# Performance work log

Measured on AMD Instinct MI355X. Metric: run time of the kernel, lower is better.

The kernel has to match this reference:

```python
import jax, jax.numpy as jnp
import numpy as np

# static config (matches init_kwargs)
B, HID, NH, D = 1, 1024, 16, 64
T, Hh, W = 8, 32, 32
TT, TH, TW = 2, 8, 8            # tile sizes (numel 128)
WT, WH, WW = 6 // TT, 16 // TH, 16 // TW  # window in tiles: 3,2,2
NTT, NTH, NTW = T // TT, Hh // TH, W // TW  # 4,4,4
NTILE = NTT * NTH * NTW          # 64
TILE = TT * TH * TW              # 128
WK = WT * WH * WW                # 12 kv tiles per q tile
S = T * Hh * W


def _dim_window(nt, w):
    left = w // 2
    right = w // 2 + (w % 2) - 1
    center = jnp.clip(jnp.arange(nt), left, nt - 1 - right)
    return center[:, None] - left + jnp.arange(w)  # [nt, w]


def _kv_tile_idx():
    kt = _dim_window(NTT, WT)  # [NTT, WT]
    kh = _dim_window(NTH, WH)  # [NTH, WH]
    kw = _dim_window(NTW, WW)  # [NTW, WW]
    idx = (kt[:, None, None, :, None, None] * (NTH * NTW)
           + kh[None, :, None, None, :, None] * NTW
           + kw[None, None, :, None, None, :])
    return idx.reshape(NTILE, WK)


def _to_tiles(x, nh):
    # [B, S, nh*D] -> [B, nh, NTILE, TILE, D]; seq laid out (ntt tt nth th ntw tw)
    x = x.reshape(B, NTT, TT, NTH, TH, NTW, TW, nh, D)
    x = x.transpose(0, 7, 1, 3, 5, 2, 4, 6, 8)
    return x.reshape(B, nh, NTILE, TILE, D)


def _from_tiles(o):
    # [B, NH, NTILE, TILE, D] -> [B, S, NH*D]
    o = o.reshape(B, NH, NTT, NTH, NTW, TT, TH, TW, D)
    o = o.transpose(0, 2, 5, 3, 6, 4, 7, 1, 8)
    return o.reshape(B, S, NH * D)


def setup_inputs() -> dict:
    key = jax.random.key(0)
    ks = jax.random.split(key, 5)
    sc = 1.0 / np.sqrt(HID)
    return {
        'hidden_states': jax.random.normal(ks[0], (B, S, HID), jnp.float32),
        'wq': jax.random.normal(ks[1], (HID, NH * D), jnp.float32) * sc,
        'wk': jax.random.normal(ks[2], (HID, NH * D), jnp.float32) * sc,
        'wv': jax.random.normal(ks[3], (HID, NH * D), jnp.float32) * sc,
        'wo': jax.random.normal(ks[4], (NH * D, HID), jnp.float32) * sc,
    }


def reference(hidden_states, wq, wk, wv, wo):
    kv_idx = _kv_tile_idx()  # [NTILE, WK]
    q = _to_tiles(hidden_states @ wq, NH)  # [B,NH,NTILE,TILE,D]
    k = _to_tiles(hidden_states @ wk, NH)
    v = _to_tiles(hidden_states @ wv, NH)
    # gather each query tile's exact kv window (mask fully satisfied by construction)
    kg = k[:, :, kv_idx].reshape(B, NH, NTILE, WK * TILE, D)
    vg = v[:, :, kv_idx].reshape(B, NH, NTILE, WK * TILE, D)
    scores = jnp.einsum('bhnqd,bhnkd->bhnqk', q, kg) * (1.0 / np.sqrt(D))
    p = jax.nn.softmax(scores, axis=-1)
    o = jnp.einsum('bhnqk,bhnkd->bhnqd', p, vg)
    return _from_tiles(o) @ wo
```

## Files before the change

kernel.cpp:

```cpp
#include <hip/hip_runtime.h>
#include <hip/hip_bf16.h>
#include <math.h>

typedef __attribute__((ext_vector_type(8))) short          short8;
typedef __attribute__((ext_vector_type(8))) unsigned short u16x8;
typedef __attribute__((ext_vector_type(2))) unsigned int   u32x2;
typedef __attribute__((ext_vector_type(4))) float          f32x4;

#define MFMA_BF16(a, b, c) __builtin_amdgcn_mfma_f32_16x16x32_bf16((a), (b), (c), 0, 0, 0)

#define GLOAD_LDS16(gp, lp)                                        \
  __builtin_amdgcn_global_load_lds(                                \
      (const __attribute__((address_space(1))) void*)(gp),         \
      (__attribute__((address_space(3))) void*)(lp), 16, 0, 0)


__device__ __forceinline__ unsigned short f2bf(float f) {
  union { float f; unsigned int u; } v; v.f = f;
  unsigned int r = v.u + 0x7fffu + ((v.u >> 16) & 1u);
  return (unsigned short)(r >> 16);
}
__device__ __forceinline__ unsigned int pack2bf(float a, float b) {
  union { float f; unsigned int u; } x, y; x.f = a; y.f = b;
  return ((x.u + 0x8000u) >> 16) | ((y.u + 0x8000u) & 0xffff0000u);
}

__device__ __forceinline__ int row_to_seq(int r) {
  int tile = r >> 7, pos = r & 127;
  int ntt = tile >> 4, nth = (tile >> 2) & 3, ntw = tile & 3;
  int tt  = pos >> 6,  th  = (pos >> 3) & 7,  tw  = pos & 7;
  return ((ntt * 2 + tt) << 10) | ((nth * 8 + th) << 5) | (ntw * 8 + tw);
}

__global__ __launch_bounds__(256) void permute_hs(const float* __restrict__ in,
                                                  unsigned short* __restrict__ out) {
  int cid = blockIdx.x * 256 + threadIdx.x;
  int r = cid >> 7, c = (cid & 127) * 8;
  int s = row_to_seq(r);
  const float* f = in + (size_t)s * 1024 + c;
  u16x8 v;
#pragma unroll
  for (int j = 0; j < 8; ++j) v[j] = f2bf(f[j]);
  *(u16x8*)(out + (size_t)r * 1024 + c) = v;
}

__global__ __launch_bounds__(256) void transpose_w(const float* __restrict__ w0,
                                                   const float* __restrict__ w1,
                                                   const float* __restrict__ w2,
                                                   const float* __restrict__ w3,
                                                   unsigned short* __restrict__ out) {
  __shared__ unsigned short Lt[64 * 68];
  int m = blockIdx.y;
  const float* W = (m == 0) ? w0 : (m == 1) ? w1 : (m == 2) ? w2 : w3;
  unsigned short* O = out + (size_t)m * 1048576;
  int k0 = (blockIdx.x >> 4) * 64, n0 = (blockIdx.x & 15) * 64;
  int tid = threadIdx.x;
#pragma unroll
  for (int i = 0; i < 2; ++i) {
    int cid = i * 256 + tid;
    int kr = cid >> 3, c = cid & 7;
    const float* f = W + (size_t)(k0 + kr) * 1024 + n0 + c * 8;
#pragma unroll
    for (int j = 0; j < 8; ++j) Lt[(c * 8 + j) * 68 + kr] = f2bf(f[j]);
  }
  __syncthreads();
#pragma unroll
  for (int i = 0; i < 2; ++i) {
    int cid = i * 256 + tid;
    int nr = cid >> 3, c = cid & 7;
    u16x8 v;
#pragma unroll
    for (int j = 0; j < 8; ++j) v[j] = Lt[nr * 68 + c * 8 + j];
    *(u16x8*)(O + (size_t)(n0 + nr) * 1024 + k0 + c * 8) = v;
  }
}

template <int SCATTER, int OUT_F32>
__device__ __forceinline__ void gemm_bt_body(const unsigned short* __restrict__ A,
                                             const unsigned short* __restrict__ Bt,
                                             void* __restrict__ Cv,
                                             int row0, int col0, float scale) {
  __shared__ unsigned short As[128 * 64];
  __shared__ unsigned short Bs[128 * 64];
  const int tid  = threadIdx.x;
  const int lane = tid & 63, w = tid >> 6;
  const int quad = lane >> 4, lm = lane & 15;
  const int wr = (w >> 1) * 64, wc = (w & 1) * 64;
  f32x4 acc[4][4] = {};
  for (int kt = 0; kt < 16; ++kt) {
    const int k0 = kt * 64;
    __syncthreads();
#pragma unroll
    for (int i = 0; i < 4; ++i) {
      int cid = i * 256 + tid;
      int r = cid >> 3, c = cid & 7;
      int cg = c ^ (r & 7);
      int base = (i * 256 + (tid & 192)) * 8;
      GLOAD_LDS16(A  + (size_t)(row0 + r) * 1024 + k0 + cg * 8, As + base);
      GLOAD_LDS16(Bt + (size_t)(col0 + r) * 1024 + k0 + cg * 8, Bs + base);
    }
    __syncthreads();
#pragma unroll
    for (int kh = 0; kh < 2; ++kh) {
      short8 af[4], bf[4];
#pragma unroll
      for (int t = 0; t < 4; ++t) {
        int ca = (kh * 4 + quad) ^ (lm & 7);
        af[t] = *(const short8*)(As + (wr + t * 16 + lm) * 64 + ca * 8);
        bf[t] = *(const short8*)(Bs + (wc + t * 16 + lm) * 64 + ca * 8);
      }
#pragma unroll
      for (int rt = 0; rt < 4; ++rt)
#pragma unroll
        for (int ct = 0; ct < 4; ++ct)
          acc[rt][ct] = MFMA_BF16(af[rt], bf[ct], acc[rt][ct]);
    }
  }
#pragma unroll
  for (int rt = 0; rt < 4; ++rt)
#pragma unroll
    for (int ct = 0; ct < 4; ++ct)
#pragma unroll
      for (int g = 0; g < 4; ++g) {
        int R  = row0 + wr + rt * 16 + quad * 4 + g;
        int Cc = col0 + wc + ct * 16 + lm;
        int Rs = SCATTER ? row_to_seq(R) : R;
        float vv = acc[rt][ct][g] * scale;
        if (OUT_F32) ((float*)Cv)[(size_t)Rs * 1024 + Cc] = vv;
        else ((unsigned short*)Cv)[(size_t)Rs * 1024 + Cc] = f2bf(vv);
      }
}

__global__ __launch_bounds__(256) void gemm_qkv(const unsigned short* __restrict__ A,
                                                const unsigned short* __restrict__ Wt,
                                                unsigned short* __restrict__ QKV) {
  float scale = (blockIdx.z == 0) ? 0.18033688011112042f : 1.0f;
  gemm_bt_body<0, 0>(A, Wt + (size_t)blockIdx.z * 1048576,
                     QKV + (size_t)blockIdx.z * 8388608,
                     blockIdx.y * 128, blockIdx.x * 128, scale);
}

__global__ __launch_bounds__(256) void gemm_out(const unsigned short* __restrict__ A,
                                                const unsigned short* __restrict__ Wt,
                                                float* __restrict__ Cout) {
  gemm_bt_body<1, 1>(A, Wt, Cout, blockIdx.y * 128, blockIdx.x * 128, 1.0f);
}

__global__ __launch_bounds__(256) void transpose_v(const unsigned short* __restrict__ V,
                                                   unsigned short* __restrict__ Vt) {
  __shared__ unsigned short Lt[64 * 136];
  int kt = blockIdx.x, h = blockIdx.y, tid = threadIdx.x;
#pragma unroll
  for (int i = 0; i < 4; ++i) {
    int cid = i * 256 + tid;
    int r = cid >> 3, c = cid & 7;
    u16x8 v = *(const u16x8*)(V + (size_t)(kt * 128 + r) * 1024 + h * 64 + c * 8);
#pragma unroll
    for (int j = 0; j < 8; ++j) Lt[(c * 8 + j) * 136 + r] = v[j];
  }
  __syncthreads();
#pragma unroll
  for (int i = 0; i < 4; ++i) {
    int cid = i * 256 + tid;
    int d = cid >> 4, c = cid & 15;
    u16x8 v = *(const u16x8*)(Lt + d * 136 + c * 8);
    *(u16x8*)(Vt + (size_t)(h * 64 + d) * 8192 + kt * 128 + c * 8) = v;
  }
}

__global__ __launch_bounds__(512, 4) void attn(const unsigned short* __restrict__ Q,
                                               const unsigned short* __restrict__ K,
                                               const unsigned short* __restrict__ Vt,
                                               unsigned short* __restrict__ O) {
  __shared__ unsigned short Ks[128 * 64];
  __shared__ unsigned short Vs[64 * 128];
  __shared__ unsigned short Pb[8 * 16 * 64];

  const int tid  = threadIdx.x;
  const int lane = tid & 63, w = tid >> 6;
  const int quad = lane >> 4, lm = lane & 15;
  unsigned short* Pbw = Pb + w * 1024;

  const int h = blockIdx.x >> 6, qt = blockIdx.x & 63;
  const int ntt = qt >> 4, nth = (qt >> 2) & 3, ntw = qt & 3;
  const int kt0 = min(max(ntt, 1), 2) - 1;
  const int kh0 = min(max(nth, 1), 3) - 1;
  const int kw0 = min(max(ntw, 1), 3) - 1;

  short8 bq[2];
#pragma unroll
  for (int kh = 0; kh < 2; ++kh)
    bq[kh] = *(const short8*)(Q + (size_t)(qt * 128 + w * 16 + lm) * 1024
                                + h * 64 + kh * 32 + quad * 8);

  short8 ones8;
#pragma unroll
  for (int j = 0; j < 8; ++j) ones8[j] = (short)0x3F80;

  f32x4 o_acc[4] = {};
  f32x4 l_acc = {};

  {
    const int kvt0 = kt0 * 16 + kh0 * 4 + kw0;
#pragma unroll
    for (int i = 0; i < 2; ++i) {
      int cid = i * 512 + tid;
      int r = cid >> 3, c = cid & 7, cg = c ^ (r & 7);
      int base = (i * 512 + (tid & 448)) * 8;
      GLOAD_LDS16(K + (size_t)(kvt0 * 128 + r) * 1024 + h * 64 + cg * 8, Ks + base);
    }
  }
  __syncthreads();

  for (int it = 0; it < 12; ++it) {
    const int tt2 = it >> 2, hh2 = (it >> 1) & 1, ww2 = it & 1;
    const int kvt = (kt0 + tt2) * 16 + (kh0 + hh2) * 4 + (kw0 + ww2);

#pragma unroll
    for (int i = 0; i < 2; ++i) {
      int cid = i * 512 + tid;
      int d = cid >> 4, c = cid & 15, cg = c ^ (d & 7);
      int base = (i * 512 + (tid & 448)) * 8;
      GLOAD_LDS16(Vt + (size_t)(h * 64 + d) * 8192 + kvt * 128 + cg * 8, Vs + base);
    }

    f32x4 sa[8] = {};
#pragma unroll
    for (int kh = 0; kh < 2; ++kh) {
      short8 ak[8];
#pragma unroll
      for (int rt = 0; rt < 8; ++rt)
        ak[rt] = *(const short8*)(Ks + (rt * 16 + lm) * 64 + (((kh * 4 + quad) ^ (lm & 7)) * 8));
#pragma unroll
      for (int rt = 0; rt < 8; ++rt)
        sa[rt] = MFMA_BF16(ak[rt], bq[kh], sa[rt]);
    }

    u32x2 pk[8];
#pragma unroll
    for (int rt = 0; rt < 8; ++rt) {
      pk[rt][0] = pack2bf(exp2f(sa[rt][0]), exp2f(sa[rt][1]));
      pk[rt][1] = pack2bf(exp2f(sa[rt][2]), exp2f(sa[rt][3]));
    }

    __syncthreads();

    if (it < 11) {
      const int jt = it + 1;
      const int t2 = jt >> 2, h2 = (jt >> 1) & 1, w2 = jt & 1;
      const int kvn = (kt0 + t2) * 16 + (kh0 + h2) * 4 + (kw0 + w2);
#pragma unroll
      for (int i = 0; i < 2; ++i) {
        int cid = i * 512 + tid;
        int r = cid >> 3, c = cid & 7, cg = c ^ (r & 7);
        int base = (i * 512 + (tid & 448)) * 8;
        GLOAD_LDS16(K + (size_t)(kvn * 128 + r) * 1024 + h * 64 + cg * 8, Ks + base);
      }
    }

#pragma unroll
    for (int half = 0; half < 2; ++half) {
#pragma unroll
      for (int rt4 = 0; rt4 < 4; ++rt4) {
        *(u32x2*)(Pbw + lm * 64 + (((rt4 * 2 + (quad >> 1)) ^ (lm & 7)) * 8) + (quad & 1) * 4)
            = pk[half * 4 + rt4];
      }
#pragma unroll
      for (int ks2 = 0; ks2 < 2; ++ks2) {
        short8 ap = *(const short8*)(Pbw + lm * 64 + (((ks2 * 4 + quad) ^ (lm & 7)) * 8));
        l_acc = MFMA_BF16(ap, ones8, l_acc);
        const int ks = half * 2 + ks2;
#pragma unroll
        for (int nt = 0; nt < 4; ++nt) {
          short8 bv = *(const short8*)(Vs + (nt * 16 + lm) * 128 + (((ks * 4 + quad) ^ (lm & 7)) * 8));
          o_acc[nt] = MFMA_BF16(ap, bv, o_acc[nt]);
        }
      }
    }

    __syncthreads();
  }

#pragma unroll
  for (int g = 0; g < 4; ++g) {
    float inv = 1.0f / l_acc[g];
#pragma unroll
    for (int nt = 0; nt < 4; ++nt) {
      int R = qt * 128 + w * 16 + quad * 4 + g;
      O[(size_t)R * 1024 + h * 64 + nt * 16 + lm] = f2bf(o_acc[nt][g] * inv);
    }
  }
}

extern "C" void kernel_launch(void* const* d_in, const int* in_sizes, int n_in,
                              void* d_out, int out_size, void* d_ws, size_t ws_size,
                              hipStream_t stream) {
  const float* hs = (const float*)d_in[0];
  const float* wq = (const float*)d_in[1];
  const float* wk = (const float*)d_in[2];
  const float* wv = (const float*)d_in[3];
  const float* wo = (const float*)d_in[4];
  float* out = (float*)d_out;

  const size_t NEL = 8388608;
  unsigned short* ws  = (unsigned short*)d_ws;
  unsigned short* HSt = ws;
  unsigned short* Qb  = ws + 1 * NEL;
  unsigned short* Kb  = ws + 2 * NEL;
  unsigned short* Vb  = ws + 3 * NEL;
  unsigned short* Vtb = ws + 4 * NEL;
  unsigned short* Ot  = ws + 5 * NEL;
  unsigned short* Wt  = ws + 6 * NEL;
  if (ws_size < (6 * NEL + 4 * 1048576) * sizeof(unsigned short)) return;

  permute_hs<<<4096, 256, 0, stream>>>(hs, HSt);
  transpose_w<<<dim3(256, 4), 256, 0, stream>>>(wq, wk, wv, wo, Wt);
  gemm_qkv<<<dim3(8, 64, 3), 256, 0, stream>>>(HSt, Wt, Qb);
  transpose_v<<<dim3(64, 16), 256, 0, stream>>>(Vb, Vtb);
  attn<<<1024, 512, 0, stream>>>(Qb, Kb, Vtb, Ot);
  gemm_out<<<dim3(8, 64, 1), 256, 0, stream>>>(Ot, Wt + 3 * 1048576, out);
  (void)in_sizes; (void)n_in; (void)out_size;
}
```

Before: 293.1 us.

## Use hardware bf16 pack, precompute load offsets, add MFMA priority hints

Replaces the manual float-to-bf16 packing with the v_cvt_pk_bf16_f32 instruction. Global-to-LDS load addresses for K and Vt are hoisted into per-thread offsets computed once, so the loop adds only a shifted tile index. s_setprio hints are wrapped around the MFMA issues so that waves doing matrix math get scheduling priority. The packing instruction rounds differently from the old add-0x8000 truncation, and the fine-grained setprio toggles may disturb the instruction schedule.

```diff
diff --git a/kernel.cpp b/kernel.cpp
--- a/kernel.cpp
+++ b/kernel.cpp
@@ -21,8 +21,9 @@
   return (unsigned short)(r >> 16);
 }
 __device__ __forceinline__ unsigned int pack2bf(float a, float b) {
-  union { float f; unsigned int u; } x, y; x.f = a; y.f = b;
-  return ((x.u + 0x8000u) >> 16) | ((y.u + 0x8000u) & 0xffff0000u);
+  unsigned int r;
+  asm("v_cvt_pk_bf16_f32 %0, %1, %2" : "=v"(r) : "v"(a), "v"(b));
+  return r;
 }
 
 __device__ __forceinline__ int row_to_seq(int r) {
@@ -187,6 +188,18 @@
   const int kh0 = min(max(nth, 1), 3) - 1;
   const int kw0 = min(max(ntw, 1), 3) - 1;
 
+  const int cid1 = 512 + tid;
+  const int rK0 = tid  >> 3, cgK0 = (tid  & 7) ^ (rK0 & 7);
+  const int rK1 = cid1 >> 3, cgK1 = (cid1 & 7) ^ (rK1 & 7);
+  const unsigned koff0 = rK0 * 1024 + h * 64 + cgK0 * 8;
+  const unsigned koff1 = rK1 * 1024 + h * 64 + cgK1 * 8;
+  const int dV0 = tid  >> 4, cgV0 = (tid  & 15) ^ (dV0 & 7);
+  const int dV1 = cid1 >> 4, cgV1 = (cid1 & 15) ^ (dV1 & 7);
+  const unsigned voff0 = (h * 64 + dV0) * 8192 + cgV0 * 8;
+  const unsigned voff1 = (h * 64 + dV1) * 8192 + cgV1 * 8;
+  const unsigned ldsD0 = (tid & 448) * 8;
+  const unsigned ldsD1 = (512 + (tid & 448)) * 8;
+
   short8 bq[2];
 #pragma unroll
   for (int kh = 0; kh < 2; ++kh)
@@ -201,14 +214,9 @@
   f32x4 l_acc = {};
 
   {
-    const int kvt0 = kt0 * 16 + kh0 * 4 + kw0;
-#pragma unroll
-    for (int i = 0; i < 2; ++i) {
-      int cid = i * 512 + tid;
-      int r = cid >> 3, c = cid & 7, cg = c ^ (r & 7);
-      int base = (i * 512 + (tid & 448)) * 8;
-      GLOAD_LDS16(K + (size_t)(kvt0 * 128 + r) * 1024 + h * 64 + cg * 8, Ks + base);
-    }
+    const unsigned k0 = (unsigned)(kt0 * 16 + kh0 * 4 + kw0) << 17;
+    GLOAD_LDS16(K + koff0 + k0, Ks + ldsD0);
+    GLOAD_LDS16(K + koff1 + k0, Ks + ldsD1);
   }
   __syncthreads();
 
@@ -216,12 +224,10 @@
     const int tt2 = it >> 2, hh2 = (it >> 1) & 1, ww2 = it & 1;
     const int kvt = (kt0 + tt2) * 16 + (kh0 + hh2) * 4 + (kw0 + ww2);
 
-#pragma unroll
-    for (int i = 0; i < 2; ++i) {
-      int cid = i * 512 + tid;
-      int d = cid >> 4, c = cid & 15, cg = c ^ (d & 7);
-      int base = (i * 512 + (tid & 448)) * 8;
-      GLOAD_LDS16(Vt + (size_t)(h * 64 + d) * 8192 + kvt * 128 + cg * 8, Vs + base);
+    {
+      const unsigned v0 = (unsigned)kvt << 7;
+      GLOAD_LDS16(Vt + voff0 + v0, Vs + ldsD0);
+      GLOAD_LDS16(Vt + voff1 + v0, Vs + ldsD1);
     }
 
     f32x4 sa[8] = {};
@@ -231,9 +237,11 @@
 #pragma unroll
       for (int rt = 0; rt < 8; ++rt)
         ak[rt] = *(const short8*)(Ks + (rt * 16 + lm) * 64 + (((kh * 4 + quad) ^ (lm & 7)) * 8));
+      __builtin_amdgcn_s_setprio(1);
 #pragma unroll
       for (int rt = 0; rt < 8; ++rt)
         sa[rt] = MFMA_BF16(ak[rt], bq[kh], sa[rt]);
+      __builtin_amdgcn_s_setprio(0);
     }
 
     u32x2 pk[8];
@@ -248,14 +256,9 @@
     if (it < 11) {
       const int jt = it + 1;
       const int t2 = jt >> 2, h2 = (jt >> 1) & 1, w2 = jt & 1;
-      const int kvn = (kt0 + t2) * 16 + (kh0 + h2) * 4 + (kw0 + w2);
-#pragma unroll
-      for (int i = 0; i < 2; ++i) {
-        int cid = i * 512 + tid;
-        int r = cid >> 3, c = cid & 7, cg = c ^ (r & 7);
-        int base = (i * 512 + (tid & 448)) * 8;
-        GLOAD_LDS16(K + (size_t)(kvn * 128 + r) * 1024 + h * 64 + cg * 8, Ks + base);
-      }
+      const unsigned kn = (unsigned)((kt0 + t2) * 16 + (kh0 + h2) * 4 + (kw0 + w2)) << 17;
+      GLOAD_LDS16(K + koff0 + kn, Ks + ldsD0);
+      GLOAD_LDS16(K + koff1 + kn, Ks + ldsD1);
     }
 
 #pragma unroll
@@ -268,12 +271,16 @@
 #pragma unroll
       for (int ks2 = 0; ks2 < 2; ++ks2) {
         short8 ap = *(const short8*)(Pbw + lm * 64 + (((ks2 * 4 + quad) ^ (lm & 7)) * 8));
+        const int ks = half * 2 + ks2;
+        __builtin_amdgcn_s_setprio(1);
         l_acc = MFMA_BF16(ap, ones8, l_acc);
-        const int ks = half * 2 + ks2;
+        __builtin_amdgcn_s_setprio(0);
 #pragma unroll
         for (int nt = 0; nt < 4; ++nt) {
           short8 bv = *(const short8*)(Vs + (nt * 16 + lm) * 128 + (((ks * 4 + quad) ^ (lm & 7)) * 8));
+          __builtin_amdgcn_s_setprio(1);
           o_acc[nt] = MFMA_BF16(ap, bv, o_acc[nt]);
+          __builtin_amdgcn_s_setprio(0);
         }
       }
     }
```

After: 284.0 us. 3.1% less time.
